# Kernel optimization log

Hardware: AMD Instinct MI355X
Metric: run time of the kernel (lower is better)

Reference implementation:

```python
import jax, jax.numpy as jnp
import numpy as np

N = 10000    # nodes
D = 128      # d_model
K = 16       # d_state
S = 5        # seq_len (tokens per node)
E = 320000   # edges
R = 200      # num relation types
P = E // (S - 1)  # edges sampled per tokenizer step
EPS = 1e-5


def setup_inputs() -> dict:
    key = jax.random.key(0)
    ks = jax.random.split(key, 16)
    sc = 1.0 / np.sqrt(D)
    return {
        "x": jax.random.normal(ks[0], (N, D), jnp.float32),
        "edge_index": jax.random.randint(ks[1], (2, E), 0, N),
        "edge_type": jax.random.randint(ks[2], (E,), 0, R),
        "perms": jax.random.randint(ks[3], (S - 1, P), 0, E),
        "rel_table": jax.random.normal(ks[4], (R, D), jnp.float32) * 0.1,
        "log_A": jax.random.normal(ks[5], (D, K), jnp.float32) * 0.1,
        "W_B": jax.random.normal(ks[6], (D, K), jnp.float32) * sc,
        "W_C": jax.random.normal(ks[7], (D, K), jnp.float32) * sc,
        "W_delta": jax.random.normal(ks[8], (D, D), jnp.float32) * sc,
        "b_delta": jnp.zeros((D,), jnp.float32),
        "W_g": jax.random.normal(ks[9], (D, D), jnp.float32) * sc,
        "b_g": jnp.zeros((D,), jnp.float32),
        "W_out": jax.random.normal(ks[10], (D, D), jnp.float32) * sc,
        "b_out": jnp.zeros((D,), jnp.float32),
        "ln_g": jnp.ones((D,), jnp.float32),
        "ln_b": jnp.zeros((D,), jnp.float32),
    }


def _tokenize(x, edge_index, edge_type, perms, rel_table):
    # x: [N,D]; perms: [S-1,P] -> tokens [N,S,D]
    src, dst = edge_index[0], edge_index[1]
    step_src = src[perms]                    # [S-1,P]
    step_dst = dst[perms]                    # [S-1,P]
    msg = x[step_src] + rel_table[edge_type[perms]]  # [S-1,P,D]
    seg = jax.vmap(lambda i, m: jax.ops.segment_sum(m, i, num_segments=N))(step_dst, msg)  # [S-1,N,D]
    deg = jax.vmap(lambda i: jax.ops.segment_sum(jnp.ones((P,), x.dtype), i, num_segments=N))(step_dst)  # [S-1,N]
    neigh = seg / jnp.clip(deg, 1.0)[..., None]
    return jnp.concatenate([x[:, None, :], jnp.moveaxis(neigh, 0, 1)], axis=1)  # [N,S,D]


def _selective_scan(tokens, log_A, W_B, W_C, W_delta, b_delta):
    # tokens: [N,S,D] -> [N,S,D]
    deltas = jax.nn.softplus(tokens @ W_delta + b_delta)  # [N,S,D]
    Bs = tokens @ W_B                                     # [N,S,K]
    Cs = tokens @ W_C                                     # [N,S,K]
    A_cont = -jnp.exp(log_A)                              # [D,K]
    A_disc = jnp.exp(deltas[..., None] * A_cont)          # [N,S,D,K]
    Bx = deltas[..., None] * Bs[:, :, None, :] * tokens[..., None]  # [N,S,D,K] = B_disc * x_k

    def step(state, xs):
        a, bx, c = xs                          # [N,D,K],[N,D,K],[N,K]
        state = a * state + bx
        y = jnp.einsum('ndk,nk->nd', state, c)
        return state, y

    init = jnp.zeros((tokens.shape[0], D, K), tokens.dtype)
    _, ys = jax.lax.scan(step, init, (jnp.moveaxis(A_disc, 1, 0),
                                      jnp.moveaxis(Bx, 1, 0),
                                      jnp.moveaxis(Cs, 1, 0)))
    return jnp.moveaxis(ys, 0, 1)  # [N,S,D]


def reference(x, edge_index, edge_type, perms, rel_table, log_A, W_B, W_C,
              W_delta, b_delta, W_g, b_g, W_out, b_out, ln_g, ln_b):
    tokens = _tokenize(x, edge_index, edge_type, perms, rel_table)
    out_f = _selective_scan(tokens, log_A, W_B, W_C, W_delta, b_delta)
    out_b = _selective_scan(tokens[:, ::-1, :], log_A, W_B, W_C, W_delta, b_delta)
    scan_out = (out_f + out_b[:, ::-1, :]).mean(axis=1)  # [N,D]
    gate = jax.nn.silu(x @ W_g + b_g)
    res = x + gate * (scan_out @ W_out + b_out)
    mu = res.mean(axis=-1, keepdims=True)
    var = res.var(axis=-1, keepdims=True)
    return (res - mu) / jnp.sqrt(var + EPS) * ln_g + ln_b
```

## Files before the change

kernel.cpp:

```cpp
#include <hip/hip_runtime.h>
#include <hip/hip_bf16.h>
#include <math.h>

#define N_NODES 10000
#define D_MODEL 128
#define E_EDGES 320000
#define P_EDGES 80000
#define LN_EPS 1e-5f
#define CAP 32
#define NCOLS 160
#define NT 16

typedef __attribute__((ext_vector_type(8))) short bf16x8;
typedef __attribute__((ext_vector_type(4))) float f32x4;

#if __has_builtin(__builtin_amdgcn_exp2f)
#define EXP2(x) __builtin_amdgcn_exp2f(x)
#else
#define EXP2(x) exp2f(x)
#endif
#define LOG2E 1.44269504088896f

__device__ __forceinline__ unsigned short f2bf(float f) {
    __hip_bfloat16 h = __float2bfloat16(f);
    return *reinterpret_cast<unsigned short*>(&h);
}
__device__ __forceinline__ float bf2f(unsigned int u) {
    return __uint_as_float(u << 16);
}

__global__ __launch_bounds__(256) void prep_all(
    const float* __restrict__ Wd, const float* __restrict__ Wb,
    const float* __restrict__ Wc, const float* __restrict__ Wg,
    const float* __restrict__ W_out,
    const float* __restrict__ x, const float* __restrict__ rel,
    const int* __restrict__ edge_index, const int* __restrict__ edge_type,
    const int* __restrict__ perms,
    unsigned short* __restrict__ Bp, unsigned short* __restrict__ Wop,
    unsigned short* __restrict__ Wgp,
    unsigned short* __restrict__ x_bf, unsigned short* __restrict__ rel_bf,
    int* __restrict__ cnt, int2* __restrict__ slots,
    unsigned short* __restrict__ tokens)
{
    int gid = blockIdx.x * 256 + threadIdx.x;
    if (gid < 20480) {
        int k = gid / NCOLS, n = gid - (gid / NCOLS) * NCOLS;
        float v;
        if (n < 128)      v = Wd[k * 128 + n];
        else if (n < 144) v = Wb[k * 16 + (n - 128)];
        else              v = Wc[k * 16 + (n - 144)];
        Bp[((size_t)(k >> 3) * NCOLS + n) * 8 + (k & 7)] = f2bf(v);
    } else if (gid < 36864) {
        int i = gid - 20480;
        int k = i >> 7, n = i & 127;
        Wop[((size_t)(k >> 3) * 128 + n) * 8 + (k & 7)] = f2bf(W_out[k * 128 + n]);
    } else if (gid < 53248) {
        int i = gid - 36864;
        int k = i >> 7, n = i & 127;
        Wgp[((size_t)(k >> 3) * 128 + n) * 8 + (k & 7)] = f2bf(Wg[k * 128 + n]);
    } else if (gid < 78848) {
        int i = gid - 53248;
        rel_bf[i] = f2bf(rel[i]);
    } else if (gid < 1358848) {
        int i = gid - 78848;
        unsigned short v = f2bf(x[i]);
        x_bf[i] = v;
        tokens[(size_t)(i >> 7) * 640 + (i & 127)] = v;
    } else if (gid < 1678848) {
        int i = gid - 1358848;
        int s = i / P_EDGES;
        int e = perms[i];
        int src = edge_index[e];
        int dst = edge_index[E_EDGES + e];
        int ty  = edge_type[e];
        int b = dst * 4 + s;
        int pos = atomicAdd(&cnt[b], 1);
        if (pos < CAP) slots[(size_t)b * CAP + pos] = make_int2(src, ty);
    }
}

__global__ __launch_bounds__(256) void gather_tokens(
    const unsigned short* __restrict__ x_bf,
    const int* __restrict__ cnt, const int2* __restrict__ slots,
    const unsigned short* __restrict__ rel_bf,
    unsigned short* __restrict__ tokens)
{
    int n = blockIdx.x;
    int w = threadIdx.x >> 6, lane = threadIdx.x & 63;
    int b = n * 4 + w;
    int c = cnt[b];
    int cc = c < CAP ? c : CAP;
    const int2* sl = slots + (size_t)b * CAP;
    const unsigned int* xu = (const unsigned int*)x_bf;
    const unsigned int* ru = (const unsigned int*)rel_bf;
    float ax = 0.f, ay = 0.f;
    int j = 0;
    for (; j + 4 <= cc; j += 4) {
        int4 e01 = *(const int4*)(sl + j);
        int4 e23 = *(const int4*)(sl + j + 2);
        unsigned int x0 = xu[(size_t)e01.x * 64 + lane];
        unsigned int r0 = ru[(size_t)e01.y * 64 + lane];
        unsigned int x1 = xu[(size_t)e01.z * 64 + lane];
        unsigned int r1 = ru[(size_t)e01.w * 64 + lane];
        unsigned int x2 = xu[(size_t)e23.x * 64 + lane];
        unsigned int r2 = ru[(size_t)e23.y * 64 + lane];
        unsigned int x3 = xu[(size_t)e23.z * 64 + lane];
        unsigned int r3 = ru[(size_t)e23.w * 64 + lane];
        ax += (bf2f(x0 & 0xffffu) + bf2f(r0 & 0xffffu))
            + (bf2f(x1 & 0xffffu) + bf2f(r1 & 0xffffu))
            + (bf2f(x2 & 0xffffu) + bf2f(r2 & 0xffffu))
            + (bf2f(x3 & 0xffffu) + bf2f(r3 & 0xffffu));
        ay += (bf2f(x0 >> 16) + bf2f(r0 >> 16))
            + (bf2f(x1 >> 16) + bf2f(r1 >> 16))
            + (bf2f(x2 >> 16) + bf2f(r2 >> 16))
            + (bf2f(x3 >> 16) + bf2f(r3 >> 16));
    }
    if (j + 2 <= cc) {
        int4 e01 = *(const int4*)(sl + j);
        unsigned int x0 = xu[(size_t)e01.x * 64 + lane];
        unsigned int r0 = ru[(size_t)e01.y * 64 + lane];
        unsigned int x1 = xu[(size_t)e01.z * 64 + lane];
        unsigned int r1 = ru[(size_t)e01.w * 64 + lane];
        ax += (bf2f(x0 & 0xffffu) + bf2f(r0 & 0xffffu))
            + (bf2f(x1 & 0xffffu) + bf2f(r1 & 0xffffu));
        ay += (bf2f(x0 >> 16) + bf2f(r0 >> 16))
            + (bf2f(x1 >> 16) + bf2f(r1 >> 16));
        j += 2;
    }
    if (j < cc) {
        int2 se = sl[j];
        unsigned int xa = xu[(size_t)se.x * 64 + lane];
        unsigned int ra = ru[(size_t)se.y * 64 + lane];
        ax += bf2f(xa & 0xffffu) + bf2f(ra & 0xffffu);
        ay += bf2f(xa >> 16) + bf2f(ra >> 16);
    }
    float inv = 1.f / fmaxf((float)c, 1.f);
    unsigned int pack = (unsigned int)f2bf(ax * inv)
                      | ((unsigned int)f2bf(ay * inv) << 16);
    ((unsigned int*)tokens)[((size_t)n * 5 + w + 1) * 64 + lane] = pack;
}

__global__ __launch_bounds__(512, 4) void mega(
    const unsigned short* __restrict__ tokens,
    const unsigned short* __restrict__ Bp,
    const unsigned short* __restrict__ Wop,
    const unsigned short* __restrict__ Wgp,
    const unsigned short* __restrict__ x_bf,
    const float* __restrict__ x,
    const float* __restrict__ log_A,
    const float* __restrict__ b_delta, const float* __restrict__ b_g,
    const float* __restrict__ b_out,
    const float* __restrict__ ln_g, const float* __restrict__ ln_b,
    float* __restrict__ out)
{
    const int tid = threadIdx.x;
    const int wv = tid >> 6, lane = tid & 63;
    const int quad = lane >> 4, l16 = lane & 15;
    const int m0 = blockIdx.x * 80;
    const int n0 = blockIdx.x * NT;

    __shared__ __align__(16) char smem[47104];
    unsigned short* s_deltaT = (unsigned short*)smem;
    float*          s_bcf    = (float*)(smem + 32768);
    unsigned short* s_so     = (unsigned short*)(smem + 43008);
    float* s_res  = (float*)smem;
    float* s_pmu  = (float*)(smem + 8448);
    float* s_pv2  = (float*)(smem + 9472);
    float* s_mu   = (float*)(smem + 10496);
    float* s_rstd = (float*)(smem + 10560);

    for (int u = wv; u < 25; u += 8) {
        int f = u / 5, tp = u - (u / 5) * 5;
        f32x4 acc0 = {0.f, 0.f, 0.f, 0.f};
        f32x4 acc1 = {0.f, 0.f, 0.f, 0.f};
        const unsigned short* arow =
            tokens + (size_t)(m0 + f * 16 + l16) * 128 + quad * 8;
        #pragma unroll
        for (int kc = 0; kc < 128; kc += 32) {
            bf16x8 a = *(const bf16x8*)(arow + kc);
            bf16x8 b0 = *(const bf16x8*)(Bp +
                ((size_t)(kc / 8 + quad) * NCOLS + 16 * (2 * tp) + l16) * 8);
            bf16x8 b1 = *(const bf16x8*)(Bp +
                ((size_t)(kc / 8 + quad) * NCOLS + 16 * (2 * tp + 1) + l16) * 8);
            acc0 = __builtin_amdgcn_mfma_f32_16x16x32_bf16(a, b0, acc0, 0, 0, 0);
            acc1 = __builtin_amdgcn_mfma_f32_16x16x32_bf16(a, b1, acc1, 0, 0, 0);
        }
        int rbase = f * 16 + quad * 4;
        #pragma unroll
        for (int half = 0; half < 2; ++half) {
            int t = 2 * tp + half;
            int c = 16 * t + l16;
            #pragma unroll
            for (int reg = 0; reg < 4; ++reg) {
                int r = rbase + reg;
                float v = half ? acc1[reg] : acc0[reg];
                if (t < 8) {
                    float z = v + b_delta[c];
                    float d = (z > 15.f) ? z : log1pf(__expf(z));
                    int nd = r / 5, sx = r - nd * 5;
                    s_deltaT[nd * 1024 + c * 8 + sx] = f2bf(d);
                } else {
                    s_bcf[r * 32 + (c - 128)] = v;
                }
            }
        }
    }
    __syncthreads();

    {
        const int lane32 = lane & 31;
        const int khalf  = lane >> 5;
        const int dim    = ((wv & 3) << 5) | lane32;
        const int parity = wv >> 2;
        float Ac[8];
        {
            const float4* la = (const float4*)(log_A + dim * 16 + khalf * 8);
            float4 lv0 = la[0], lv1 = la[1];
            Ac[0] = -__expf(lv0.x) * LOG2E;
            Ac[1] = -__expf(lv0.y) * LOG2E;
            Ac[2] = -__expf(lv0.z) * LOG2E;
            Ac[3] = -__expf(lv0.w) * LOG2E;
            Ac[4] = -__expf(lv1.x) * LOG2E;
            Ac[5] = -__expf(lv1.y) * LOG2E;
            Ac[6] = -__expf(lv1.z) * LOG2E;
            Ac[7] = -__expf(lv1.w) * LOG2E;
        }
        #pragma unroll 1
        for (int i = 0; i < 4; ++i) {
            int nA = parity + 4 * i;
            int nB = nA + 2;
            const float* bcA = s_bcf + nA * 160 + khalf * 8;
            const float* bcB = s_bcf + nB * 160 + khalf * 8;
            float tvA[5], tvB[5];
            {
                const unsigned short* tbA =
                    tokens + (size_t)(n0 + nA) * 640 + dim;
                const unsigned short* tbB =
                    tokens + (size_t)(n0 + nB) * 640 + dim;
                #pragma unroll
                for (int s = 0; s < 5; ++s) {
                    tvA[s] = bf2f(tbA[s * 128]);
                    tvB[s] = bf2f(tbB[s * 128]);
                }
            }
            bf16x8 dpkA = *(const bf16x8*)(s_deltaT + nA * 1024 + dim * 8);
            bf16x8 dpkB = *(const bf16x8*)(s_deltaT + nB * 1024 + dim * 8);
            const unsigned short* dvA = (const unsigned short*)&dpkA;
            const unsigned short* dvB = (const unsigned short*)&dpkB;
            float stA[8], VA[8], stB[8], VB[8];
            #pragma unroll
            for (int k = 0; k < 8; ++k) { stA[k] = 0.f; stB[k] = 0.f; }
            float totalA = 0.f, totalB = 0.f;
            #pragma unroll
            for (int s = 0; s < 5; ++s) {
                float dlA = bf2f(dvA[s]), dlB = bf2f(dvB[s]);
                float dtvA = dlA * tvA[s], dtvB = dlB * tvB[s];
                f32x4 BA0 = *(const f32x4*)(bcA + s * 32);
                f32x4 BA1 = *(const f32x4*)(bcA + s * 32 + 4);
                f32x4 CA0 = *(const f32x4*)(bcA + s * 32 + 16);
                f32x4 CA1 = *(const f32x4*)(bcA + s * 32 + 20);
                f32x4 BB0 = *(const f32x4*)(bcB + s * 32);
                f32x4 BB1 = *(const f32x4*)(bcB + s * 32 + 4);
                f32x4 CB0 = *(const f32x4*)(bcB + s * 32 + 16);
                f32x4 CB1 = *(const f32x4*)(bcB + s * 32 + 20);
                float yfA = 0.f, ubA = 0.f, yfB = 0.f, ubB = 0.f;
                #pragma unroll
                for (int k = 0; k < 8; ++k) {
                    float Ba = (k < 4) ? BA0[k] : BA1[k - 4];
                    float Ca = (k < 4) ? CA0[k] : CA1[k - 4];
                    float Bb = (k < 4) ? BB0[k] : BB1[k - 4];
                    float Cb = (k < 4) ? CB0[k] : CB1[k - 4];
                    float VsA = (s == 0) ? Ca : VA[k] + Ca;
                    float VsB = (s == 0) ? Cb : VB[k] + Cb;
                    float eA = EXP2(dlA * Ac[k]);
                    float eB = EXP2(dlB * Ac[k]);
                    stA[k] = fmaf(eA, stA[k], dtvA * Ba);
                    stB[k] = fmaf(eB, stB[k], dtvB * Bb);
                    yfA = fmaf(stA[k], Ca, yfA);
                    yfB = fmaf(stB[k], Cb, yfB);
                    ubA = fmaf(VsA, Ba, ubA);
                    ubB = fmaf(VsB, Bb, ubB);
                    VA[k] = eA * VsA;
                    VB[k] = eB * VsB;
                }
                totalA += yfA + dtvA * ubA;
                totalB += yfB + dtvB * ubB;
            }
            totalA += __shfl_xor(totalA, 32, 64);
            totalB += __shfl_xor(totalB, 32, 64);
            if (khalf == 0) {
                s_so[nA * 128 + (((dim >> 3) ^ (nA & 7)) << 3) + (dim & 7)] =
                    f2bf(totalA * 0.2f);
                s_so[nB * 128 + (((dim >> 3) ^ (nB & 7)) << 3) + (dim & 7)] =
                    f2bf(totalB * 0.2f);
            }
        }
    }
    __syncthreads();

    {
        f32x4 accO = {0,0,0,0};
        f32x4 accG = {0,0,0,0};
        const unsigned short* grow = x_bf + (size_t)(n0 + l16) * 128 + quad * 8;
        #pragma unroll
        for (int kc = 0; kc < 128; kc += 32) {
            bf16x8 a = *(const bf16x8*)(s_so + l16 * 128 +
                           (((kc / 8 + quad) ^ (l16 & 7)) << 3));
            bf16x8 ag = *(const bf16x8*)(grow + kc);
            size_t bi = ((size_t)(kc / 8 + quad) * 128 + 16 * wv + l16) * 8;
            bf16x8 bo = *(const bf16x8*)(Wop + bi);
            bf16x8 bg = *(const bf16x8*)(Wgp + bi);
            accO = __builtin_amdgcn_mfma_f32_16x16x32_bf16(a,  bo, accO, 0, 0, 0);
            accG = __builtin_amdgcn_mfma_f32_16x16x32_bf16(ag, bg, accG, 0, 0, 0);
        }

        {
            int c = wv * 16 + l16;
            #pragma unroll
            for (int reg = 0; reg < 4; ++reg) {
                int lrow = quad * 4 + reg;
                float o  = accO[reg] + b_out[c];
                float gl = accG[reg] + b_g[c];
                float gate = gl / (1.f + __expf(-gl));
                s_res[lrow * 132 + c] = x[(size_t)(n0 + lrow) * 128 + c] + gate * o;
            }
        }
        __syncthreads();

        if (tid < 256) {
            int row = tid >> 4, q = tid & 15;
            float s = 0.f, s2 = 0.f;
            #pragma unroll
            for (int i = 0; i < 8; ++i) {
                float vv = s_res[row * 132 + q + 16 * i];
                s += vv; s2 += vv * vv;
            }
            s_pmu[row * 16 + q] = s; s_pv2[row * 16 + q] = s2;
        }
        __syncthreads();
        if (tid < 16) {
            float s = 0.f, s2 = 0.f;
            #pragma unroll
            for (int i = 0; i < 16; ++i) { s += s_pmu[tid * 16 + i]; s2 += s_pv2[tid * 16 + i]; }
            float mu = s * (1.f / 128.f);
            float var = s2 * (1.f / 128.f) - mu * mu;
            s_mu[tid] = mu;
            s_rstd[tid] = rsqrtf(var + LN_EPS);
        }
        __syncthreads();
        #pragma unroll
        for (int i = 0; i < 4; ++i) {
            int idx = i * 512 + tid;
            int row = idx >> 7, c = idx & 127;
            out[(size_t)(n0 + row) * 128 + c] =
                (s_res[row * 132 + c] - s_mu[row]) * s_rstd[row] * ln_g[c] + ln_b[c];
        }
    }
}

extern "C" void kernel_launch(void* const* d_in, const int* in_sizes, int n_in,
                              void* d_out, int out_size, void* d_ws, size_t ws_size,
                              hipStream_t stream) {
    const float* x          = (const float*)d_in[0];
    const int*   edge_index = (const int*)  d_in[1];
    const int*   edge_type  = (const int*)  d_in[2];
    const int*   perms      = (const int*)  d_in[3];
    const float* rel_table  = (const float*)d_in[4];
    const float* log_A      = (const float*)d_in[5];
    const float* W_B        = (const float*)d_in[6];
    const float* W_C        = (const float*)d_in[7];
    const float* W_delta    = (const float*)d_in[8];
    const float* b_delta    = (const float*)d_in[9];
    const float* W_g        = (const float*)d_in[10];
    const float* b_g        = (const float*)d_in[11];
    const float* W_out      = (const float*)d_in[12];
    const float* b_out      = (const float*)d_in[13];
    const float* ln_g       = (const float*)d_in[14];
    const float* ln_b       = (const float*)d_in[15];

    char* ws = (char*)d_ws;
    int*            cnt    = (int*)           (ws + 0);
    unsigned short* Bp     = (unsigned short*)(ws + 163840);
    unsigned short* Wop    = (unsigned short*)(ws + 204800);
    unsigned short* Wgp    = (unsigned short*)(ws + 237568);
    unsigned short* x_bf   = (unsigned short*)(ws + 270336);
    unsigned short* rel_bf = (unsigned short*)(ws + 2830336);
    unsigned short* tokens = (unsigned short*)(ws + 2881536);
    int2*           slots  = (int2*)          (ws + 15683584);

    (void)hipMemsetAsync(cnt, 0, 163840, stream);

    prep_all<<<6558, 256, 0, stream>>>(
        W_delta, W_B, W_C, W_g, W_out, x, rel_table, edge_index, edge_type,
        perms, Bp, Wop, Wgp, x_bf, rel_bf, cnt, slots, tokens);

    gather_tokens<<<N_NODES, 256, 0, stream>>>(
        x_bf, cnt, slots, rel_bf, tokens);

    mega<<<N_NODES / NT, 512, 0, stream>>>(
        tokens, Bp, Wop, Wgp, x_bf, x, log_A, b_delta, b_g, b_out,
        ln_g, ln_b, (float*)d_out);
}
```

Baseline: 204.7 us.

## Stage token tile in swizzled LDS and reuse it for projection GEMM and scan

Each block now copies its 80x128 bf16 token tile from global memory into LDS once, with an XOR swizzle to avoid bank conflicts. Both the MFMA projection GEMM (A operand) and the scan's per-token value loads read from that copy instead of making separate global reads. The GEMM is also split into 50 single-accumulator units, and log1pf is replaced by the faster __logf(1+exp). LDS use grows from 47104 to 67584 bytes and launch bounds drop from 4 to 2 blocks per CU, which can reduce occupancy.

```diff
diff --git a/kernel.cpp b/kernel.cpp
--- a/kernel.cpp
+++ b/kernel.cpp
@@ -140,7 +140,7 @@
     ((unsigned int*)tokens)[((size_t)n * 5 + w + 1) * 64 + lane] = pack;
 }
 
-__global__ __launch_bounds__(512, 4) void mega(
+__global__ __launch_bounds__(512, 2) void mega(
     const unsigned short* __restrict__ tokens,
     const unsigned short* __restrict__ Bp,
     const unsigned short* __restrict__ Wop,
@@ -159,49 +159,56 @@
     const int m0 = blockIdx.x * 80;
     const int n0 = blockIdx.x * NT;
 
-    __shared__ __align__(16) char smem[47104];
-    unsigned short* s_deltaT = (unsigned short*)smem;
-    float*          s_bcf    = (float*)(smem + 32768);
-    unsigned short* s_so     = (unsigned short*)(smem + 43008);
+    __shared__ __align__(16) char smem[67584];
+    unsigned short* s_deltaT = (unsigned short*)(smem + 20480);
+    float*          s_bcf    = (float*)(smem + 53248);
+    unsigned short* s_so     = (unsigned short*)(smem + 63488);
     float* s_res  = (float*)smem;
     float* s_pmu  = (float*)(smem + 8448);
     float* s_pv2  = (float*)(smem + 9472);
     float* s_mu   = (float*)(smem + 10496);
     float* s_rstd = (float*)(smem + 10560);
 
-    for (int u = wv; u < 25; u += 8) {
-        int f = u / 5, tp = u - (u / 5) * 5;
-        f32x4 acc0 = {0.f, 0.f, 0.f, 0.f};
-        f32x4 acc1 = {0.f, 0.f, 0.f, 0.f};
-        const unsigned short* arow =
-            tokens + (size_t)(m0 + f * 16 + l16) * 128 + quad * 8;
+    {
+        const uint4* gsrc = (const uint4*)(tokens + (size_t)m0 * 128);
+        #pragma unroll
+        for (int p = 0; p < 3; ++p) {
+            int idx = p * 512 + tid;
+            if (idx < 1280) {
+                uint4 v = gsrc[idx];
+                int swz = (idx * 16) ^ (((idx >> 4) & 7) << 4);
+                *(uint4*)(smem + swz) = v;
+            }
+        }
+    }
+    __syncthreads();
+
+    for (int u = wv; u < 50; u += 8) {
+        int f = u / 10, t = u - (u / 10) * 10;
+        f32x4 acc = {0.f, 0.f, 0.f, 0.f};
+        const int arow_l = f * 16 + l16;
+        const int abase  = arow_l * 256 + quad * 16;
+        const int aswz   = (arow_l & 7) << 4;
         #pragma unroll
         for (int kc = 0; kc < 128; kc += 32) {
-            bf16x8 a = *(const bf16x8*)(arow + kc);
-            bf16x8 b0 = *(const bf16x8*)(Bp +
-                ((size_t)(kc / 8 + quad) * NCOLS + 16 * (2 * tp) + l16) * 8);
-            bf16x8 b1 = *(const bf16x8*)(Bp +
-                ((size_t)(kc / 8 + quad) * NCOLS + 16 * (2 * tp + 1) + l16) * 8);
-            acc0 = __builtin_amdgcn_mfma_f32_16x16x32_bf16(a, b0, acc0, 0, 0, 0);
-            acc1 = __builtin_amdgcn_mfma_f32_16x16x32_bf16(a, b1, acc1, 0, 0, 0);
+            bf16x8 a = *(const bf16x8*)(smem + ((abase + kc * 2) ^ aswz));
+            bf16x8 b = *(const bf16x8*)(Bp +
+                ((size_t)(kc / 8 + quad) * NCOLS + 16 * t + l16) * 8);
+            acc = __builtin_amdgcn_mfma_f32_16x16x32_bf16(a, b, acc, 0, 0, 0);
         }
         int rbase = f * 16 + quad * 4;
+        int c = 16 * t + l16;
         #pragma unroll
-        for (int half = 0; half < 2; ++half) {
-            int t = 2 * tp + half;
-            int c = 16 * t + l16;
-            #pragma unroll
-            for (int reg = 0; reg < 4; ++reg) {
-                int r = rbase + reg;
-                float v = half ? acc1[reg] : acc0[reg];
-                if (t < 8) {
-                    float z = v + b_delta[c];
-                    float d = (z > 15.f) ? z : log1pf(__expf(z));
-                    int nd = r / 5, sx = r - nd * 5;
-                    s_deltaT[nd * 1024 + c * 8 + sx] = f2bf(d);
-                } else {
-                    s_bcf[r * 32 + (c - 128)] = v;
-                }
+        for (int reg = 0; reg < 4; ++reg) {
+            int r = rbase + reg;
+            float v = acc[reg];
+            if (t < 8) {
+                float z = v + b_delta[c];
+                float d = (z > 15.f) ? z : __logf(1.f + __expf(z));
+                int nd = r / 5, sx = r - nd * 5;
+                s_deltaT[nd * 1024 + c * 8 + sx] = f2bf(d);
+            } else {
+                s_bcf[r * 32 + (c - 128)] = v;
             }
         }
     }
@@ -229,24 +236,21 @@
         for (int i = 0; i < 4; ++i) {
             int nA = parity + 4 * i;
             int nB = nA + 2;
-            const float* bcA = s_bcf + nA * 160 + khalf * 8;
-            const float* bcB = s_bcf + nB * 160 + khalf * 8;
             float tvA[5], tvB[5];
-            {
-                const unsigned short* tbA =
-                    tokens + (size_t)(n0 + nA) * 640 + dim;
-                const unsigned short* tbB =
-                    tokens + (size_t)(n0 + nB) * 640 + dim;
-                #pragma unroll
-                for (int s = 0; s < 5; ++s) {
-                    tvA[s] = bf2f(tbA[s * 128]);
-                    tvB[s] = bf2f(tbB[s * 128]);
-                }
+            #pragma unroll
+            for (int s = 0; s < 5; ++s) {
+                int rA = nA * 5 + s, rB = nB * 5 + s;
+                tvA[s] = bf2f(*(const unsigned short*)(smem +
+                            ((rA * 256 + dim * 2) ^ ((rA & 7) << 4))));
+                tvB[s] = bf2f(*(const unsigned short*)(smem +
+                            ((rB * 256 + dim * 2) ^ ((rB & 7) << 4))));
             }
             bf16x8 dpkA = *(const bf16x8*)(s_deltaT + nA * 1024 + dim * 8);
             bf16x8 dpkB = *(const bf16x8*)(s_deltaT + nB * 1024 + dim * 8);
             const unsigned short* dvA = (const unsigned short*)&dpkA;
             const unsigned short* dvB = (const unsigned short*)&dpkB;
+            const float* bcA = s_bcf + nA * 160 + khalf * 8;
+            const float* bcB = s_bcf + nB * 160 + khalf * 8;
             float stA[8], VA[8], stB[8], VB[8];
             #pragma unroll
             for (int k = 0; k < 8; ++k) { stA[k] = 0.f; stB[k] = 0.f; }
```

Measured after the change: 191.9 us. 1.07x faster.
